# Kernel optimization log

Hardware: AMD Instinct MI355X
Metric: run time of the kernel (lower is better)

Reference implementation:

```python
import jax, jax.numpy as jnp
import numpy as np

TILES = 8           # OpenCV createCLAHE default tileGridSize=(8,8)
CLIP_LIMIT = 1.2    # module init arg


def _clahe(img, clip_limit=CLIP_LIMIT, tiles=TILES):
    """CLAHE on a [C,H,W] float image in [0,1]; H,W divisible by `tiles`."""
    C, H, W = img.shape
    th, tw = H // tiles, W // tiles
    area = th * tw
    clip = max(int(clip_limit * area / 256.0), 1)  # OpenCV clip-limit scaling

    # Quantize to 8-bit bins (matches (img*255).astype(uint8) truncation)
    v = jnp.clip((img * 255.0).astype(jnp.int32), 0, 255)        # [C,H,W]

    # ---- per-tile, per-channel 256-bin histogram via segment_sum ----
    ty = jnp.arange(H) // th
    tx = jnp.arange(W) // tw
    tile = ty[:, None] * tiles + tx[None, :]                      # [H,W]
    seg = (jnp.arange(C)[:, None, None] * (tiles * tiles) + tile[None]) * 256 + v
    hist = jax.ops.segment_sum(
        jnp.ones((C * H * W,), jnp.float32), seg.reshape(-1),
        num_segments=C * tiles * tiles * 256,
    ).reshape(C, tiles, tiles, 256)

    # ---- clip + uniform redistribution of excess ----
    clipped = jnp.minimum(hist, jnp.float32(clip))
    excess = (hist - clipped).sum(-1, keepdims=True)
    clipped = clipped + excess / 256.0

    # ---- CDF -> per-tile LUT ----
    cdf = jnp.cumsum(clipped, axis=-1)
    lut = jnp.clip(jnp.round(cdf * (255.0 / area)), 0.0, 255.0)  # [C,T,T,256]

    # ---- bilinear interpolation between the 4 neighboring tile LUTs ----
    fy = (jnp.arange(H, dtype=jnp.float32) + 0.5) / th - 0.5
    fx = (jnp.arange(W, dtype=jnp.float32) + 0.5) / tw - 0.5
    y0 = jnp.clip(jnp.floor(fy), 0, tiles - 1).astype(jnp.int32)
    x0 = jnp.clip(jnp.floor(fx), 0, tiles - 1).astype(jnp.int32)
    ay = jnp.clip(fy - y0.astype(jnp.float32), 0.0, 1.0)
    ax = jnp.clip(fx - x0.astype(jnp.float32), 0.0, 1.0)
    y1 = jnp.minimum(y0 + 1, tiles - 1)
    x1 = jnp.minimum(x0 + 1, tiles - 1)

    ci = jnp.arange(C)[:, None, None]
    Y0, Y1 = y0[None, :, None], y1[None, :, None]
    X0, X1 = x0[None, None, :], x1[None, None, :]
    g00 = lut[ci, Y0, X0, v]
    g01 = lut[ci, Y0, X1, v]
    g10 = lut[ci, Y1, X0, v]
    g11 = lut[ci, Y1, X1, v]

    wy = ay[None, :, None]
    wx = ax[None, None, :]
    top = g00 * (1.0 - wx) + g01 * wx
    bot = g10 * (1.0 - wx) + g11 * wx
    out = top * (1.0 - wy) + bot * wy
    return (out / 255.0).astype(jnp.float32)


def setup_inputs() -> dict:
    key = jax.random.key(0)
    img = jax.random.uniform(key, (3, 4096, 4096), dtype=jnp.float32)
    return {"img": img}


def reference(img):
    # Deterministic baseline: always apply CLAHE (the p-gated identity branch
    # of the torch module is trivial and excluded for correctness testing).
    return _clahe(img)
```

## Files before the change

### kernel.cpp

```cpp
#include <hip/hip_runtime.h>
#include <stdint.h>

#define TILES 8
#define HH 4096
#define WW 4096
#define CC 3
#define TH 512
#define TW 512
#define AREA (TH * TW)
#define CLIPV 1228u

__global__ __launch_bounds__(256) void clahe_hist_kernel(
    const float* __restrict__ img,
    uint32_t* __restrict__ vpack,
    int store_v,
    uint32_t* __restrict__ hist)
{
    __shared__ uint32_t sh[4 * 264];
    const int tid  = threadIdx.x;
    const int wave = tid >> 6;
    uint32_t* myh  = sh + wave * 264;

    for (int i = tid; i < 4 * 264; i += 256) sh[i] = 0;
    __syncthreads();

    const int bid = blockIdx.x;
    const int sub = bid & 15;
    const int tl  = bid >> 4;
    const int tx  = tl & 7;
    const int ty  = (tl >> 3) & 7;
    const int c   = tl >> 6;

    const size_t base = ((size_t)c * HH + (size_t)(ty * TH + sub * 32)) * WW + (size_t)tx * TW;

    for (int it = 0; it < 4; ++it) {
        const int i0 = it * 1024 + tid;
        size_t addr[4];
        float4 p[4];
#pragma unroll
        for (int j = 0; j < 4; ++j) {
            const int s  = i0 + j * 256;
            const int rl = s >> 7;
            const int c4 = s & 127;
            addr[j] = base + (size_t)rl * WW + (size_t)c4 * 4;
            p[j] = *(const float4*)(img + addr[j]);
        }
#pragma unroll
        for (int j = 0; j < 4; ++j) {
            int v0 = min(max((int)(p[j].x * 255.0f), 0), 255);
            int v1 = min(max((int)(p[j].y * 255.0f), 0), 255);
            int v2 = min(max((int)(p[j].z * 255.0f), 0), 255);
            int v3 = min(max((int)(p[j].w * 255.0f), 0), 255);

            atomicAdd(&myh[v0], 1u);
            atomicAdd(&myh[v1], 1u);
            atomicAdd(&myh[v2], 1u);
            atomicAdd(&myh[v3], 1u);

            if (store_v) {
                uint32_t pk = (uint32_t)v0 | ((uint32_t)v1 << 8) |
                              ((uint32_t)v2 << 16) | ((uint32_t)v3 << 24);
                vpack[addr[j] >> 2] = pk;
            }
        }
    }
    __syncthreads();

    const uint32_t s = sh[tid] + sh[264 + tid] + sh[528 + tid] + sh[792 + tid];
    atomicAdd(&hist[(size_t)tl * 256 + tid], s);
}

__global__ __launch_bounds__(256) void clahe_lut_kernel(
    const uint32_t* __restrict__ hist,
    float* __restrict__ lut)
{
    __shared__ uint32_t exs[4];
    __shared__ float wsum[4];

    const int tid  = threadIdx.x;
    const int wave = tid >> 6;
    const int lane = tid & 63;
    const int blk  = blockIdx.x;

    const uint32_t h  = hist[(size_t)blk * 256 + tid];
    const uint32_t cl = min(h, CLIPV);
    uint32_t ex = h - cl;

#pragma unroll
    for (int d = 32; d > 0; d >>= 1) ex += __shfl_down(ex, d, 64);
    if (lane == 0) exs[wave] = ex;
    __syncthreads();
    const uint32_t extot = exs[0] + exs[1] + exs[2] + exs[3];

    float x = (float)cl + (float)extot * (1.0f / 256.0f);

#pragma unroll
    for (int d = 1; d < 64; d <<= 1) {
        float t = __shfl_up(x, d, 64);
        if (lane >= d) x += t;
    }
    if (lane == 63) wsum[wave] = x;
    __syncthreads();
    float add = 0.0f;
    for (int w = 0; w < wave; ++w) add += wsum[w];
    const float cdf = x + add;

    float l = rintf(cdf * (255.0f / (float)AREA));
    l = fminf(fmaxf(l, 0.0f), 255.0f);
    lut[(size_t)blk * 256 + tid] = l;
}

__global__ __launch_bounds__(256) void clahe_apply_kernel(
    const float* __restrict__ img,
    const uint32_t* __restrict__ vpack,
    const float* __restrict__ lut,
    float* __restrict__ out,
    int use_v)
{
    __shared__ float rb[TILES * 256];

    const int b = blockIdx.x;
    const int g = b & 511;
    const int c = b >> 9;
    const int ybase = g * 8;
    const int tid = threadIdx.x;

    const float fyb = ((float)ybase + 0.5f) * (1.0f / (float)TH) - 0.5f;
    int y0 = (int)floorf(fyb);
    y0 = min(max(y0, 0), TILES - 1);
    const int y1 = min(y0 + 1, TILES - 1);

    const float* lr0 = lut + ((size_t)(c * TILES + y0) * TILES) * 256;
    const float* lr1 = lut + ((size_t)(c * TILES + y1) * TILES) * 256;

    float a0[8], a1[8];
#pragma unroll
    for (int k = 0; k < 8; ++k) {
        a0[k] = lr0[k * 256 + tid];
        a1[k] = lr1[k * 256 + tid];
    }

    const float4* img4 = (const float4*)img;
    float4* out4 = (float4*)out;

    for (int r = 0; r < 8; ++r) {
        const int y = ybase + r;
        const float fy = ((float)y + 0.5f) * (1.0f / (float)TH) - 0.5f;
        const float ay = fminf(fmaxf(fy - (float)y0, 0.0f), 1.0f);

        if (r) __syncthreads();
#pragma unroll
        for (int k = 0; k < 8; ++k)
            rb[k * 256 + tid] = a0[k] + ay * (a1[k] - a0[k]);
        __syncthreads();

        const size_t rowbase = ((size_t)c * HH + (size_t)y) * (WW / 4);

#pragma unroll
        for (int s = 0; s < 4; ++s) {
            const int slot = s * 256 + tid;

            uint32_t pv = 0;
            float4 p = make_float4(0.f, 0.f, 0.f, 0.f);
            if (use_v) pv = vpack[rowbase + slot];
            else       p  = img4[rowbase + slot];

            const int xbase = slot * 4;
            const float fx0 = ((float)xbase + 0.5f) * (1.0f / (float)TW) - 0.5f;
            int x0 = (int)floorf(fx0);
            x0 = min(max(x0, 0), TILES - 1);
            const int x1 = min(x0 + 1, TILES - 1);
            const float* r0 = rb + x0 * 256;
            const float* r1 = rb + x1 * 256;
            const float fxr = fx0 - (float)x0;

            float res[4];
#pragma unroll
            for (int k = 0; k < 4; ++k) {
                int v;
                if (use_v) {
                    v = (int)((pv >> (8 * k)) & 255u);
                } else {
                    const float pk = (k == 0) ? p.x : (k == 1) ? p.y : (k == 2) ? p.z : p.w;
                    v = min(max((int)(pk * 255.0f), 0), 255);
                }
                const float ax = fminf(fmaxf(fxr + (float)k * (1.0f / (float)TW), 0.0f), 1.0f);
                const float g0 = r0[v];
                const float g1 = r1[v];
                res[k] = (g0 + ax * (g1 - g0)) * (1.0f / 255.0f);
            }
            out4[rowbase + slot] = make_float4(res[0], res[1], res[2], res[3]);
        }
    }
}

extern "C" void kernel_launch(void* const* d_in, const int* in_sizes, int n_in,
                              void* d_out, int out_size, void* d_ws, size_t ws_size,
                              hipStream_t stream)
{
    const float* img = (const float*)d_in[0];
    float* out = (float*)d_out;

    uint8_t* ws = (uint8_t*)d_ws;
    uint32_t* hist = (uint32_t*)ws;
    float*    lut  = (float*)(ws + 196608);
    uint32_t* vpack = (uint32_t*)(ws + 393216);

    const size_t need_v = 393216 + (size_t)CC * HH * WW;
    const int use_v = (ws_size >= need_v) ? 1 : 0;

    hipMemsetAsync(hist, 0, (size_t)CC * 64 * 256 * sizeof(uint32_t), stream);

    clahe_hist_kernel<<<CC * 64 * 16, 256, 0, stream>>>(img, vpack, use_v, hist);
    clahe_lut_kernel<<<CC * 64, 256, 0, stream>>>(hist, lut);
    clahe_apply_kernel<<<CC * 512, 256, 0, stream>>>(img, vpack, lut, out, use_v);
}
```

Measured before the change: 375.6 us.

## Drop hist memset via partial histograms, one-row apply blocks, nontemporal IO

The histogram kernel now writes per-block partial histograms that the LUT kernel sums, which removes the memset and the global atomics. The apply kernel now uses one block per row (12288 blocks instead of 1536). Each block issues its pixel loads up front, before building the interpolated LUT row in shared memory. Image loads and output stores use nontemporal hints. The trade-off is a larger partial-histogram buffer and redundant LUT-row interpolation per row, in exchange for more parallelism and latency overlap.

```diff
diff --git a/kernel.cpp b/kernel.cpp
--- a/kernel.cpp
+++ b/kernel.cpp
@@ -10,11 +10,13 @@
 #define AREA (TH * TW)
 #define CLIPV 1228u
 
+typedef float f4 __attribute__((ext_vector_type(4)));
+
 __global__ __launch_bounds__(256) void clahe_hist_kernel(
     const float* __restrict__ img,
     uint32_t* __restrict__ vpack,
     int store_v,
-    uint32_t* __restrict__ hist)
+    uint32_t* __restrict__ hist_part)
 {
     __shared__ uint32_t sh[4 * 264];
     const int tid  = threadIdx.x;
@@ -31,26 +33,28 @@
     const int ty  = (tl >> 3) & 7;
     const int c   = tl >> 6;
 
-    const size_t base = ((size_t)c * HH + (size_t)(ty * TH + sub * 32)) * WW + (size_t)tx * TW;
+    const size_t base4 = ((size_t)c * HH + (size_t)(ty * TH + sub * 32)) * (WW / 4)
+                       + (size_t)tx * (TW / 4);
+    const f4* img4 = (const f4*)img;
 
     for (int it = 0; it < 4; ++it) {
         const int i0 = it * 1024 + tid;
         size_t addr[4];
-        float4 p[4];
+        f4 p[4];
 #pragma unroll
         for (int j = 0; j < 4; ++j) {
             const int s  = i0 + j * 256;
             const int rl = s >> 7;
             const int c4 = s & 127;
-            addr[j] = base + (size_t)rl * WW + (size_t)c4 * 4;
-            p[j] = *(const float4*)(img + addr[j]);
+            addr[j] = base4 + (size_t)rl * (WW / 4) + (size_t)c4;
+            p[j] = __builtin_nontemporal_load(&img4[addr[j]]);
         }
 #pragma unroll
         for (int j = 0; j < 4; ++j) {
-            int v0 = min(max((int)(p[j].x * 255.0f), 0), 255);
-            int v1 = min(max((int)(p[j].y * 255.0f), 0), 255);
-            int v2 = min(max((int)(p[j].z * 255.0f), 0), 255);
-            int v3 = min(max((int)(p[j].w * 255.0f), 0), 255);
+            int v0 = min(max((int)(p[j][0] * 255.0f), 0), 255);
+            int v1 = min(max((int)(p[j][1] * 255.0f), 0), 255);
+            int v2 = min(max((int)(p[j][2] * 255.0f), 0), 255);
+            int v3 = min(max((int)(p[j][3] * 255.0f), 0), 255);
 
             atomicAdd(&myh[v0], 1u);
             atomicAdd(&myh[v1], 1u);
@@ -60,18 +64,18 @@
             if (store_v) {
                 uint32_t pk = (uint32_t)v0 | ((uint32_t)v1 << 8) |
                               ((uint32_t)v2 << 16) | ((uint32_t)v3 << 24);
-                vpack[addr[j] >> 2] = pk;
+                vpack[addr[j]] = pk;
             }
         }
     }
     __syncthreads();
 
     const uint32_t s = sh[tid] + sh[264 + tid] + sh[528 + tid] + sh[792 + tid];
-    atomicAdd(&hist[(size_t)tl * 256 + tid], s);
+    hist_part[(size_t)bid * 256 + tid] = s;
 }
 
 __global__ __launch_bounds__(256) void clahe_lut_kernel(
-    const uint32_t* __restrict__ hist,
+    const uint32_t* __restrict__ hist_part,
     float* __restrict__ lut)
 {
     __shared__ uint32_t exs[4];
@@ -82,7 +86,11 @@
     const int lane = tid & 63;
     const int blk  = blockIdx.x;
 
-    const uint32_t h  = hist[(size_t)blk * 256 + tid];
+    const uint32_t* hp = hist_part + (size_t)blk * 16 * 256;
+    uint32_t h = 0;
+#pragma unroll
+    for (int s = 0; s < 16; ++s) h += hp[s * 256 + tid];
+
     const uint32_t cl = min(h, CLIPV);
     uint32_t ex = h - cl;
 
@@ -119,78 +127,71 @@
 {
     __shared__ float rb[TILES * 256];
 
+    const int tid = threadIdx.x;
     const int b = blockIdx.x;
-    const int g = b & 511;
-    const int c = b >> 9;
-    const int ybase = g * 8;
-    const int tid = threadIdx.x;
-
-    const float fyb = ((float)ybase + 0.5f) * (1.0f / (float)TH) - 0.5f;
-    int y0 = (int)floorf(fyb);
+    const int y = b & (HH - 1);
+    const int c = b >> 12;
+
+    const size_t rowbase4 = ((size_t)c * HH + (size_t)y) * (WW / 4);
+    const f4* img4 = (const f4*)img;
+
+    uint32_t pv[4];
+    f4 p[4];
+    if (use_v) {
+#pragma unroll
+        for (int s = 0; s < 4; ++s) pv[s] = vpack[rowbase4 + s * 256 + tid];
+    } else {
+#pragma unroll
+        for (int s = 0; s < 4; ++s) p[s] = img4[rowbase4 + s * 256 + tid];
+    }
+
+    const float fy = ((float)y + 0.5f) * (1.0f / (float)TH) - 0.5f;
+    int y0 = (int)floorf(fy);
     y0 = min(max(y0, 0), TILES - 1);
+    const float ay = fminf(fmaxf(fy - (float)y0, 0.0f), 1.0f);
     const int y1 = min(y0 + 1, TILES - 1);
 
     const float* lr0 = lut + ((size_t)(c * TILES + y0) * TILES) * 256;
     const float* lr1 = lut + ((size_t)(c * TILES + y1) * TILES) * 256;
 
-    float a0[8], a1[8];
 #pragma unroll
     for (int k = 0; k < 8; ++k) {
-        a0[k] = lr0[k * 256 + tid];
-        a1[k] = lr1[k * 256 + tid];
-    }
-
-    const float4* img4 = (const float4*)img;
-    float4* out4 = (float4*)out;
-
-    for (int r = 0; r < 8; ++r) {
-        const int y = ybase + r;
-        const float fy = ((float)y + 0.5f) * (1.0f / (float)TH) - 0.5f;
-        const float ay = fminf(fmaxf(fy - (float)y0, 0.0f), 1.0f);
-
-        if (r) __syncthreads();
-#pragma unroll
-        for (int k = 0; k < 8; ++k)
-            rb[k * 256 + tid] = a0[k] + ay * (a1[k] - a0[k]);
-        __syncthreads();
-
-        const size_t rowbase = ((size_t)c * HH + (size_t)y) * (WW / 4);
-
-#pragma unroll
-        for (int s = 0; s < 4; ++s) {
-            const int slot = s * 256 + tid;
-
-            uint32_t pv = 0;
-            float4 p = make_float4(0.f, 0.f, 0.f, 0.f);
-            if (use_v) pv = vpack[rowbase + slot];
-            else       p  = img4[rowbase + slot];
-
-            const int xbase = slot * 4;
-            const float fx0 = ((float)xbase + 0.5f) * (1.0f / (float)TW) - 0.5f;
-            int x0 = (int)floorf(fx0);
-            x0 = min(max(x0, 0), TILES - 1);
-            const int x1 = min(x0 + 1, TILES - 1);
-            const float* r0 = rb + x0 * 256;
-            const float* r1 = rb + x1 * 256;
-            const float fxr = fx0 - (float)x0;
-
-            float res[4];
-#pragma unroll
-            for (int k = 0; k < 4; ++k) {
-                int v;
-                if (use_v) {
-                    v = (int)((pv >> (8 * k)) & 255u);
-                } else {
-                    const float pk = (k == 0) ? p.x : (k == 1) ? p.y : (k == 2) ? p.z : p.w;
-                    v = min(max((int)(pk * 255.0f), 0), 255);
-                }
-                const float ax = fminf(fmaxf(fxr + (float)k * (1.0f / (float)TW), 0.0f), 1.0f);
-                const float g0 = r0[v];
-                const float g1 = r1[v];
-                res[k] = (g0 + ax * (g1 - g0)) * (1.0f / 255.0f);
+        const int i = k * 256 + tid;
+        const float a = lr0[i];
+        const float d = lr1[i];
+        rb[i] = a + ay * (d - a);
+    }
+    __syncthreads();
+
+#pragma unroll
+    for (int s = 0; s < 4; ++s) {
+        const int slot = s * 256 + tid;
+
+        const int xbase = slot * 4;
+        const float fx0 = ((float)xbase + 0.5f) * (1.0f / (float)TW) - 0.5f;
+        int x0 = (int)floorf(fx0);
+        x0 = min(max(x0, 0), TILES - 1);
+        const int x1 = min(x0 + 1, TILES - 1);
+        const float* r0 = rb + x0 * 256;
+        const float* r1 = rb + x1 * 256;
+        const float fxr = fx0 - (float)x0;
+
+        float res[4];
+#pragma unroll
+        for (int k = 0; k < 4; ++k) {
+            int v;
+            if (use_v) {
+                v = (int)((pv[s] >> (8 * k)) & 255u);
+            } else {
+                v = min(max((int)(p[s][k] * 255.0f), 0), 255);
             }
-            out4[rowbase + slot] = make_float4(res[0], res[1], res[2], res[3]);
+            const float ax = fminf(fmaxf(fxr + (float)k * (1.0f / (float)TW), 0.0f), 1.0f);
+            const float g0 = r0[v];
+            const float g1 = r1[v];
+            res[k] = (g0 + ax * (g1 - g0)) * (1.0f / 255.0f);
         }
+        f4 o4 = { res[0], res[1], res[2], res[3] };
+        __builtin_nontemporal_store(o4, ((f4*)out) + rowbase4 + slot);
     }
 }
 
@@ -202,16 +203,14 @@
     float* out = (float*)d_out;
 
     uint8_t* ws = (uint8_t*)d_ws;
-    uint32_t* hist = (uint32_t*)ws;
-    float*    lut  = (float*)(ws + 196608);
-    uint32_t* vpack = (uint32_t*)(ws + 393216);
-
-    const size_t need_v = 393216 + (size_t)CC * HH * WW;
+    float*    lut       = (float*)ws;
+    uint32_t* hist_part = (uint32_t*)(ws + 196608);
+    uint32_t* vpack     = (uint32_t*)(ws + 196608 + 3145728);
+
+    const size_t need_v = 196608 + 3145728 + (size_t)CC * HH * WW;
     const int use_v = (ws_size >= need_v) ? 1 : 0;
 
-    hipMemsetAsync(hist, 0, (size_t)CC * 64 * 256 * sizeof(uint32_t), stream);
-
-    clahe_hist_kernel<<<CC * 64 * 16, 256, 0, stream>>>(img, vpack, use_v, hist);
-    clahe_lut_kernel<<<CC * 64, 256, 0, stream>>>(hist, lut);
-    clahe_apply_kernel<<<CC * 512, 256, 0, stream>>>(img, vpack, lut, out, use_v);
-}
+    clahe_hist_kernel<<<CC * 64 * 16, 256, 0, stream>>>(img, vpack, use_v, hist_part);
+    clahe_lut_kernel<<<CC * 64, 256, 0, stream>>>(hist_part, lut);
+    clahe_apply_kernel<<<CC * HH, 256, 0, stream>>>(img, vpack, lut, out, use_v);
+}
```

After: 335.8 us. 10.6% less time.
